# Kernel tuning notes

Hardware: AMD Instinct MI355X
Metric: run time of the kernel (lower is better)

Reference implementation:

```python
import jax, jax.numpy as jnp
import numpy as np

PI = 3.1415  # matches the literal constant in the source


def setup_inputs() -> dict:
    key = jax.random.key(0)
    nt, ns, nh = 1024, 2048, 32
    k1, k2, k3, k4, k5 = jax.random.split(key, 5)
    P = jax.random.uniform(k1, (nt, ns), dtype=jnp.float32) * 10.0           # precipitation >= 0
    T1 = jax.random.normal(k2, (nt, ns), dtype=jnp.float32) * 10.0           # daily min temp
    T2 = T1 + jax.random.uniform(k3, (nt, ns), dtype=jnp.float32) * 15.0 + 0.5  # max temp > min temp
    E = jax.random.uniform(k4, (nt, ns), dtype=jnp.float32) * 5.0            # potential ET >= 0
    w = jax.random.uniform(k5, (nh * 4,), dtype=jnp.float32, minval=-1.0, maxval=1.0)
    return {"P": P, "T1": T1, "T2": T2, "E": E, "w": w}


def reference(P, T1, T2, E, w):
    nt, ns = P.shape
    nh = w.shape[0] // 4

    # rain/snow partition. arccos argument is clipped for numerical safety; the
    # clipped region (|ratio|>1) is exactly where rP is overwritten by the masks,
    # so forward values match the original exactly.
    Ta = (T1 + T2) * 0.5
    ratio = jnp.clip((T1 + T2) / (T2 - T1), -1.0, 1.0)
    rP = 1.0 - jnp.arccos(ratio) / PI
    rP = jnp.where(T1 >= 0, 1.0, rP)
    rP = jnp.where(T2 <= 0, 0.0, rP)
    Ps = (1.0 - rP) * P   # snow
    Pl = rP * P           # liquid rain

    gm = jnp.exp(w[:nh]) + 1.0            # melt factor, [nh]
    ge = jax.nn.sigmoid(w[nh:2 * nh])     # ET gate, [nh]
    go = jax.nn.sigmoid(w[2 * nh:3 * nh]) # outflow gate, [nh]
    ga = jax.nn.softmax(w[3 * nh:])       # mixing weights (Dropout in eval mode = identity), [nh]

    def step(carry, xs):
        S0, H0 = carry                    # each [ns, nh]
        Ta_k, Ps_k, Pl_k, E_k = xs        # each [ns]
        Sm = jnp.minimum(S0, jnp.maximum(Ta_k[:, None] * gm, 0.0))  # snowmelt
        S = S0 + Ps_k[:, None]
        H = jnp.maximum(H0 + Sm + Pl_k[:, None] - E_k[:, None] * ge, 0.0)
        Q = H * go
        Y = jnp.sum(Q * ga, axis=1)       # [ns]
        return (S - Sm, H - Q), Y

    init = (jnp.zeros((ns, nh), P.dtype), jnp.zeros((ns, nh), P.dtype))
    _, Yout = jax.lax.scan(step, init, (Ta, Ps, Pl, E))
    return Yout  # [nt, ns]
```

## Files before the change

kernel.cpp:

```cpp
#include <hip/hip_runtime.h>

#define NT 1024
#define NS 2048
#define NH 32

__global__ __launch_bounds__(256, 1)
void waternet_kernel(const float* __restrict__ P,
                     const float* __restrict__ T1,
                     const float* __restrict__ T2,
                     const float* __restrict__ E,
                     const float* __restrict__ w,
                     float* __restrict__ Y)
{
    const int tid  = threadIdx.x;
    const int lane = tid & 31;
    const int grp  = tid >> 5;

    const int bid    = blockIdx.x;
    const int sChunk = (bid & 7) * 32 + (bid >> 3);
    const int s      = sChunk * 8 + grp;

    const float wm = w[lane];
    const float we = w[NH + lane];
    const float wo = w[2 * NH + lane];
    const float wa = w[3 * NH + lane];

    const float gm = expf(wm) + 1.0f;
    const float ge = 1.0f / (1.0f + expf(-we));
    const float go = 1.0f / (1.0f + expf(-wo));

    float mx = wa;
    #pragma unroll
    for (int o = 16; o; o >>= 1) mx = fmaxf(mx, __shfl_xor(mx, o));
    float ea = expf(wa - mx);
    float ssum = ea;
    #pragma unroll
    for (int o = 16; o; o >>= 1) ssum += __shfl_xor(ssum, o);
    const float ga  = ea / ssum;
    const float go1 = 1.0f - go;
    const float gq  = go * ga;

    float S  = 0.0f;
    float Hs = 0.0f;

    __shared__ float4 stage[2][8][32];
    __shared__ float  ytmp[2][8][32][33];

    size_t base = (size_t)lane * NS + s;
    float p0 = P[base], a0 = T1[base], b0 = T2[base], e0 = E[base];
    size_t bn = base + (size_t)32 * NS;
    float pg = P[bn], ag = T1[bn], bg = T2[bn], eg = E[bn];

    auto prep = [&](float p, float ta, float tb, float ee, int buf) {
        float sum   = ta + tb;
        float ratio = sum / (tb - ta);
        ratio = fminf(fmaxf(ratio, -1.0f), 1.0f);
        float rP = 1.0f - acosf(ratio) * (1.0f / 3.1415f);
        if (ta >= 0.0f) rP = 1.0f;
        if (tb <= 0.0f) rP = 0.0f;
        float Pl  = rP * p;
        float Ps  = p - Pl;
        float TaP = fmaxf(sum * 0.5f, 0.0f);
        stage[buf][grp][lane] = make_float4(TaP, Ps, Pl, ee);
    };

    prep(p0, a0, b0, e0, 0);

    for (int c = 0; c < 32; ++c) {
        float4 x[32];
        #pragma unroll
        for (int j = 0; j < 32; ++j) x[j] = stage[c & 1][grp][j];

        if (c < 31) prep(pg, ag, bg, eg, (c + 1) & 1);
        if (c < 30) {
            size_t nb = base + (size_t)(c + 2) * 32 * NS;
            pg = P[nb]; ag = T1[nb]; bg = T2[nb]; eg = E[nb];
        }

        if (c > 0) {
            const float* yr = &ytmp[(c - 1) & 1][grp][lane][0];
            float r0 = 0.f, r1 = 0.f, r2 = 0.f, r3 = 0.f;
            #pragma unroll
            for (int k = 0; k < 32; k += 4) {
                r0 += yr[k + 0];
                r1 += yr[k + 1];
                r2 += yr[k + 2];
                r3 += yr[k + 3];
            }
            Y[(size_t)((c - 1) * 32 + lane) * NS + s] = (r0 + r1) + (r2 + r3);
        }

        float* yw = &ytmp[c & 1][grp][0][lane];
        #pragma unroll
        for (int k = 0; k < 32; ++k) {
            const float4 xx = x[k];
            const float bm = xx.x * gm;
            const float pw = fmaf(-xx.w, ge, xx.z);
            const float Sm = fminf(S, bm);
            const float Sp = S + xx.y;
            const float h3 = fmaxf(Hs + (pw + Sm), 0.0f);
            S  = Sp - Sm;
            Hs = h3 * go1;
            yw[k * 33] = h3 * gq;
        }

        asm volatile("" ::: "memory");
    }

    {
        const float* yr = &ytmp[1][grp][lane][0];
        float r0 = 0.f, r1 = 0.f, r2 = 0.f, r3 = 0.f;
        #pragma unroll
        for (int k = 0; k < 32; k += 4) {
            r0 += yr[k + 0];
            r1 += yr[k + 1];
            r2 += yr[k + 2];
            r3 += yr[k + 3];
        }
        Y[(size_t)(31 * 32 + lane) * NS + s] = (r0 + r1) + (r2 + r3);
    }
}

extern "C" void kernel_launch(void* const* d_in, const int* in_sizes, int n_in,
                              void* d_out, int out_size, void* d_ws, size_t ws_size,
                              hipStream_t stream) {
    const float* P  = (const float*)d_in[0];
    const float* T1 = (const float*)d_in[1];
    const float* T2 = (const float*)d_in[2];
    const float* E  = (const float*)d_in[3];
    const float* w  = (const float*)d_in[4];
    float* Y = (float*)d_out;

    waternet_kernel<<<dim3(256), dim3(256), 0, stream>>>(P, T1, T2, E, w, Y);
}
```

Baseline: 45.74 us.

## Reduce hidden-unit outputs with DPP shuffles instead of an LDS transpose buffer

```diff
diff --git a/kernel.cpp b/kernel.cpp
--- a/kernel.cpp
+++ b/kernel.cpp
@@ -43,15 +43,14 @@
     float S  = 0.0f;
     float Hs = 0.0f;
 
-    __shared__ float4 stage[2][8][32];
-    __shared__ float  ytmp[2][8][32][33];
+    __shared__ float4 stage[8][32];
 
     size_t base = (size_t)lane * NS + s;
     float p0 = P[base], a0 = T1[base], b0 = T2[base], e0 = E[base];
     size_t bn = base + (size_t)32 * NS;
     float pg = P[bn], ag = T1[bn], bg = T2[bn], eg = E[bn];
 
-    auto prep = [&](float p, float ta, float tb, float ee, int buf) {
+    auto prep = [&](float p, float ta, float tb, float ee) {
         float sum   = ta + tb;
         float ratio = sum / (tb - ta);
         ratio = fminf(fmaxf(ratio, -1.0f), 1.0f);
@@ -61,36 +60,19 @@
         float Pl  = rP * p;
         float Ps  = p - Pl;
         float TaP = fmaxf(sum * 0.5f, 0.0f);
-        stage[buf][grp][lane] = make_float4(TaP, Ps, Pl, ee);
+        stage[grp][lane] = make_float4(TaP, Ps, Pl, ee);
     };
 
-    prep(p0, a0, b0, e0, 0);
+    prep(p0, a0, b0, e0);
+
+    const bool isLast = (lane == 31);
 
     for (int c = 0; c < 32; ++c) {
         float4 x[32];
         #pragma unroll
-        for (int j = 0; j < 32; ++j) x[j] = stage[c & 1][grp][j];
+        for (int j = 0; j < 32; ++j) x[j] = stage[grp][j];
 
-        if (c < 31) prep(pg, ag, bg, eg, (c + 1) & 1);
-        if (c < 30) {
-            size_t nb = base + (size_t)(c + 2) * 32 * NS;
-            pg = P[nb]; ag = T1[nb]; bg = T2[nb]; eg = E[nb];
-        }
-
-        if (c > 0) {
-            const float* yr = &ytmp[(c - 1) & 1][grp][lane][0];
-            float r0 = 0.f, r1 = 0.f, r2 = 0.f, r3 = 0.f;
-            #pragma unroll
-            for (int k = 0; k < 32; k += 4) {
-                r0 += yr[k + 0];
-                r1 += yr[k + 1];
-                r2 += yr[k + 2];
-                r3 += yr[k + 3];
-            }
-            Y[(size_t)((c - 1) * 32 + lane) * NS + s] = (r0 + r1) + (r2 + r3);
-        }
-
-        float* yw = &ytmp[c & 1][grp][0][lane];
+        float acc = 0.0f;
         #pragma unroll
         for (int k = 0; k < 32; ++k) {
             const float4 xx = x[k];
@@ -101,23 +83,33 @@
             const float h3 = fmaxf(Hs + (pw + Sm), 0.0f);
             S  = Sp - Sm;
             Hs = h3 * go1;
-            yw[k * 33] = h3 * gq;
+            float y = h3 * gq;
+
+            {
+                int t;
+                t = __builtin_amdgcn_update_dpp(0, __float_as_int(y), 0x111, 0xf, 0xf, false);
+                y += __int_as_float(t);
+                t = __builtin_amdgcn_update_dpp(0, __float_as_int(y), 0x112, 0xf, 0xf, false);
+                y += __int_as_float(t);
+                t = __builtin_amdgcn_update_dpp(0, __float_as_int(y), 0x114, 0xf, 0xf, false);
+                y += __int_as_float(t);
+                t = __builtin_amdgcn_update_dpp(0, __float_as_int(y), 0x118, 0xf, 0xf, false);
+                y += __int_as_float(t);
+                t = __builtin_amdgcn_update_dpp(0, __float_as_int(y), 0x142, 0xa, 0xf, false);
+                y += __int_as_float(t);
+            }
+
+            int rolled = __builtin_amdgcn_update_dpp(0, __float_as_int(acc), 0x134, 0xf, 0xf, false);
+            acc = isLast ? y : __int_as_float(rolled);
         }
 
-        asm volatile("" ::: "memory");
-    }
+        Y[(size_t)(c * 32 + lane) * NS + s] = acc;
 
-    {
-        const float* yr = &ytmp[1][grp][lane][0];
-        float r0 = 0.f, r1 = 0.f, r2 = 0.f, r3 = 0.f;
-        #pragma unroll
-        for (int k = 0; k < 32; k += 4) {
-            r0 += yr[k + 0];
-            r1 += yr[k + 1];
-            r2 += yr[k + 2];
-            r3 += yr[k + 3];
+        if (c < 31) prep(pg, ag, bg, eg);
+        if (c < 30) {
+            size_t nb = base + (size_t)(c + 2) * 32 * NS;
+            pg = P[nb]; ag = T1[nb]; bg = T2[nb]; eg = E[nb];
         }
-        Y[(size_t)(31 * 32 + lane) * NS + s] = (r0 + r1) + (r2 + r3);
     }
 }
 
```

Result: slower. 57.10 us (+24.9%).
